# Kernel tuning notes

Hardware: AMD Instinct MI355X
Metric: run time of the kernel (lower is better)

The kernel has to match this reference:

```python
import jax, jax.numpy as jnp
from jax import lax
import numpy as np

DIM = 384
HEADS = 8
MLP_HIDDEN = int(DIM * 4.0)
EPS = 1e-5


def layer_norm(x, g, b):
    m = jnp.mean(x, axis=-1, keepdims=True)
    v = jnp.mean((x - m) ** 2, axis=-1, keepdims=True)
    return (x - m) * lax.rsqrt(v + EPS) * g + b


def conv_pos_enc(x, H, W, w, b):
    # x: (B, N, C) -> depthwise 3x3 conv residual, act=Identity (cpe_act=False)
    B, N, C = x.shape
    feat = jnp.transpose(x, (0, 2, 1)).reshape(B, C, H, W)
    feat = lax.conv_general_dilated(
        feat, w, window_strides=(1, 1), padding='SAME',
        feature_group_count=C, dimension_numbers=('NCHW', 'OIHW', 'NCHW'))
    feat = feat + b[None, :, None, None]
    feat = jnp.transpose(feat.reshape(B, C, N), (0, 2, 1))
    return x + feat


def channel_attn(x, qkv_w, proj_w, proj_b):
    B, N, C = x.shape
    h = HEADS
    hd = C // h
    scale = hd ** (-0.5)
    qkv = x @ qkv_w.T                                # (B, N, 3C)
    qkv = qkv.reshape(B, N, 3, h, hd)
    qkv = jnp.transpose(qkv, (2, 0, 3, 1, 4))        # (3, B, h, N, hd)
    q, k, v = qkv[0], qkv[1], qkv[2]
    k = k * scale
    attn = jnp.einsum('bhnd,bhne->bhde', k, v)       # (B, h, hd, hd)
    attn = jax.nn.softmax(attn, axis=-1)
    out = jnp.einsum('bhde,bhne->bhnd', attn, q)     # (B, h, N, hd)
    out = jnp.transpose(out, (0, 2, 1, 3)).reshape(B, N, C)
    return out @ proj_w.T + proj_b


def mlp(x, fc1_w, fc1_b, fc2_w, fc2_b):
    h = jax.nn.gelu(x @ fc1_w.T + fc1_b, approximate=False)
    return h @ fc2_w.T + fc2_b


def setup_inputs() -> dict:
    key = jax.random.key(0)
    ks = jax.random.split(key, 12)
    C, Hd = DIM, MLP_HIDDEN
    s = 0.02
    return {
        'x': jax.random.normal(ks[0], (32, 784, C), dtype=jnp.float32),
        'H': 28,
        'W': 28,
        'cpe0_w': jax.random.normal(ks[1], (C, 1, 3, 3), dtype=jnp.float32) * s,
        'cpe0_b': jnp.zeros((C,), dtype=jnp.float32),
        'cpe1_w': jax.random.normal(ks[2], (C, 1, 3, 3), dtype=jnp.float32) * s,
        'cpe1_b': jnp.zeros((C,), dtype=jnp.float32),
        'norm1_g': jnp.ones((C,), dtype=jnp.float32),
        'norm1_b': jnp.zeros((C,), dtype=jnp.float32),
        'qkv_w': jax.random.normal(ks[3], (3 * C, C), dtype=jnp.float32) * s,
        'proj_w': jax.random.normal(ks[4], (C, C), dtype=jnp.float32) * s,
        'proj_b': jnp.zeros((C,), dtype=jnp.float32),
        'norm2_g': jnp.ones((C,), dtype=jnp.float32),
        'norm2_b': jnp.zeros((C,), dtype=jnp.float32),
        'fc1_w': jax.random.normal(ks[5], (Hd, C), dtype=jnp.float32) * s,
        'fc1_b': jnp.zeros((Hd,), dtype=jnp.float32),
        'fc2_w': jax.random.normal(ks[6], (C, Hd), dtype=jnp.float32) * s,
        'fc2_b': jnp.zeros((C,), dtype=jnp.float32),
    }


def reference(x, H, W, cpe0_w, cpe0_b, cpe1_w, cpe1_b, norm1_g, norm1_b,
              qkv_w, proj_w, proj_b, norm2_g, norm2_b,
              fc1_w, fc1_b, fc2_w, fc2_b):
    x = conv_pos_enc(x, H, W, cpe0_w, cpe0_b)
    cur = layer_norm(x, norm1_g, norm1_b)
    x = x + channel_attn(cur, qkv_w, proj_w, proj_b)
    x = conv_pos_enc(x, H, W, cpe1_w, cpe1_b)
    x = x + mlp(layer_norm(x, norm2_g, norm2_b), fc1_w, fc1_b, fc2_w, fc2_b)
    return x
```

## Files before the change

kernel.cpp:

```cpp
#include <hip/hip_runtime.h>
#include <hip/hip_bf16.h>
#include <math.h>
#include <stdint.h>

#define B_     32
#define HH_    28
#define WW_    28
#define N_     784
#define C_     384
#define M_     25088
#define HEADS_ 8
#define HD_    48
#define HID_   1536

typedef __bf16 bf16;
typedef __attribute__((ext_vector_type(8))) __bf16 bf16x8;
typedef __attribute__((ext_vector_type(4))) __bf16 bf16x4;
typedef __attribute__((ext_vector_type(4))) float f32x4;

__device__ __forceinline__ void gload_lds16(const void* g, void* l) {
    __builtin_amdgcn_global_load_lds(
        (const __attribute__((address_space(1))) unsigned int*)g,
        (__attribute__((address_space(3))) unsigned int*)(uintptr_t)l,
        16, 0, 0);
}

__device__ __forceinline__ float gelu_f(float v) {
    float u = 0.7978845608028654f * v * (1.f + 0.044715f * v * v);
    return __fdividef(v, 1.f + __expf(-2.f * u));
}

__global__ void convert4_kernel(const float* __restrict__ a, int na,
                                const float* __restrict__ b, int nb,
                                const float* __restrict__ c, int nc,
                                const float* __restrict__ d, int nd,
                                bf16* __restrict__ out) {
    int i = blockIdx.x * 256 + threadIdx.x;
    int j = i;
    const float* src;
    if (j < na) src = a + j;
    else { j -= na;
        if (j < nb) src = b + j;
        else { j -= nb;
            if (j < nc) src = c + j;
            else { j -= nc;
                if (j >= nd) return;
                src = d + j; } } }
    out[i] = (bf16)(*src);
}

__global__ void wtrans_kernel(const float* __restrict__ w0, const float* __restrict__ w1,
                              float* __restrict__ wt0, float* __restrict__ wt1) {
    int i = blockIdx.x * 256 + threadIdx.x;
    if (i >= C_ * 9) return;
    int c = i / 9, t = i - c * 9;
    wt0[t * C_ + c] = w0[i];
    wt1[t * C_ + c] = w1[i];
}

__global__ __launch_bounds__(256)
void cpe_ln_kernel(const float* __restrict__ x, const float* __restrict__ wt,
                   const float* __restrict__ bias, float* __restrict__ y,
                   const float* __restrict__ g, const float* __restrict__ beta,
                   bf16* __restrict__ lnout) {
    const int wave = threadIdx.x >> 6, lane = threadIdx.x & 63;
    const int f = blockIdx.x;
    const int row = (f & 7) * 3136 + (f >> 3) * 4 + wave;
    const int b = row / N_;
    const int n = row - b * N_;
    const int py = n / WW_, px = n - py * WW_;

    float acc[6], ctr[6];
    const float* xrow = x + (size_t)row * C_ + lane;
    #pragma unroll
    for (int j = 0; j < 6; j++) {
        acc[j] = bias[lane + j * 64];
        ctr[j] = xrow[j * 64];
    }

    if (py >= 1 && py <= 26 && px >= 1 && px <= 26) {
        const float* p = x + (size_t)(row - WW_ - 1) * C_ + lane;
        float v[9][6];
        #pragma unroll
        for (int t = 0; t < 9; t++) {
            if (t == 4) continue;
            const float* pt = p + ((t / 3) * WW_ + (t % 3)) * C_;
            #pragma unroll
            for (int j = 0; j < 6; j++) v[t][j] = pt[j * 64];
        }
        #pragma unroll
        for (int t = 0; t < 9; t++) {
            #pragma unroll
            for (int j = 0; j < 6; j++) {
                float xv = (t == 4) ? ctr[j] : v[t][j];
                acc[j] += wt[t * C_ + lane + j * 64] * xv;
            }
        }
    } else {
        #pragma unroll
        for (int t = 0; t < 9; t++) {
            int yy = py + t / 3 - 1, xx = px + t % 3 - 1;
            if (yy < 0 || yy >= HH_ || xx < 0 || xx >= WW_) continue;
            const float* pt = x + (size_t)(b * N_ + yy * WW_ + xx) * C_ + lane;
            #pragma unroll
            for (int j = 0; j < 6; j++)
                acc[j] += wt[t * C_ + lane + j * 64] * pt[j * 64];
        }
    }
    #pragma unroll
    for (int j = 0; j < 6; j++) acc[j] += ctr[j];

    float* yrow = y + (size_t)row * C_ + lane;
    #pragma unroll
    for (int j = 0; j < 6; j++) yrow[j * 64] = acc[j];

    float s = 0.f;
    #pragma unroll
    for (int j = 0; j < 6; j++) s += acc[j];
    #pragma unroll
    for (int off = 1; off < 64; off <<= 1) s += __shfl_xor(s, off, 64);
    float mean = s * (1.f / C_);
    float d[6], vs = 0.f;
    #pragma unroll
    for (int j = 0; j < 6; j++) { d[j] = acc[j] - mean; vs += d[j] * d[j]; }
    #pragma unroll
    for (int off = 1; off < 64; off <<= 1) vs += __shfl_xor(vs, off, 64);
    float rstd = rsqrtf(vs * (1.f / C_) + 1e-5f);
    bf16* lrow = lnout + (size_t)row * C_ + lane;
    #pragma unroll
    for (int j = 0; j < 6; j++) {
        int c = lane + j * 64;
        lrow[j * 64] = (bf16)(d[j] * rstd * g[c] + beta[c]);
    }
}

template<bool BIAS, bool GELU, bool RESID, bool OUTBF>
__global__ __launch_bounds__(256)
void gemm_kernel(const bf16* __restrict__ A, const bf16* __restrict__ Wt,
                 const float* __restrict__ bias, const float* __restrict__ resid,
                 void* __restrict__ outp, int M, int N, int K) {
    __shared__ __align__(16) bf16 As[3 * 4096];
    __shared__ __align__(16) bf16 Bs[3 * 4096];

    const int nbn = gridDim.x, nbm = gridDim.y;
    const int f = blockIdx.y * nbn + blockIdx.x;
    const int grp = f / (8 * nbn);
    const int rem = f - grp * 8 * nbn;
    const int rows = min(8, nbm - grp * 8);
    const int bm = (grp * 8 + rem % rows) * 128;
    const int bn = (rem / rows) * 128;

    const int t = threadIdx.x;
    const int wave = t >> 6, lane = t & 63;
    const int wm = (wave & 1) * 64, wn = (wave >> 1) * 64;
    const int quad = lane >> 4, r = lane & 15;

    const int ldrow = lane >> 2;
    const int ldcol = ((lane & 3) ^ ((lane >> 3) & 3)) * 8;
    const bf16* ga0 = A  + (size_t)(bm + wave * 32 + ldrow) * K + ldcol;
    const bf16* ga1 = ga0 + (size_t)16 * K;
    const bf16* gb0 = Wt + (size_t)(bn + wave * 32 + ldrow) * K + ldcol;
    const bf16* gb1 = gb0 + (size_t)16 * K;
    const int lbase = wave * 1024;
    const int nk = K >> 5;

    auto issue = [&](int st) {
        const int bb = (st % 3) * 4096;
        const int kk = st * 32;
        gload_lds16(ga0 + kk, &As[bb + lbase]);
        gload_lds16(ga1 + kk, &As[bb + lbase + 512]);
        gload_lds16(gb0 + kk, &Bs[bb + lbase]);
        gload_lds16(gb1 + kk, &Bs[bb + lbase + 512]);
    };

    f32x4 acc[4][4] = {};
    issue(0); issue(1);

    const int sq = (quad ^ ((r >> 1) & 3)) * 8;

    for (int s = 0; s < nk; ++s) {
        if (s + 1 < nk) asm volatile("s_waitcnt vmcnt(4)" ::: "memory");
        else            asm volatile("s_waitcnt vmcnt(0)" ::: "memory");
        asm volatile("s_barrier" ::: "memory");
        if (s + 2 < nk) issue(s + 2);

        const bf16* as = &As[(s % 3) * 4096];
        const bf16* bs = &Bs[(s % 3) * 4096];
        bf16x8 af[4], bfr[4];
        #pragma unroll
        for (int i = 0; i < 4; i++)
            af[i] = *(const bf16x8*)(&as[(wm + i * 16 + r) * 32 + sq]);
        #pragma unroll
        for (int j = 0; j < 4; j++)
            bfr[j] = *(const bf16x8*)(&bs[(wn + j * 16 + r) * 32 + sq]);
        #pragma unroll
        for (int i = 0; i < 4; i++)
            #pragma unroll
            for (int j = 0; j < 4; j++)
                acc[i][j] = __builtin_amdgcn_mfma_f32_16x16x32_bf16(bfr[j], af[i], acc[i][j], 0, 0, 0);
    }

    #pragma unroll
    for (int j = 0; j < 4; j++) {
        const int n = bn + wn + j * 16 + quad * 4;
        f32x4 bv = {};
        if (BIAS) bv = *(const f32x4*)(&bias[n]);
        #pragma unroll
        for (int i = 0; i < 4; i++) {
            const size_t m = (size_t)(bm + wm + i * 16 + r);
            f32x4 v = acc[i][j];
            if (BIAS) v += bv;
            if (GELU) {
                #pragma unroll
                for (int e = 0; e < 4; e++) v[e] = gelu_f(v[e]);
            }
            if (RESID) v += *(const f32x4*)(&resid[m * N + n]);
            if (OUTBF) {
                bf16x4 ov;
                #pragma unroll
                for (int e = 0; e < 4; e++) ov[e] = (bf16)v[e];
                *(bf16x4*)((bf16*)outp + m * N + n) = ov;
            } else {
                *(f32x4*)((float*)outp + m * N + n) = v;
            }
        }
    }
}

__global__ __launch_bounds__(256)
void attn_fused_kernel(const bf16* __restrict__ qkvb, bf16* __restrict__ outp) {
    __shared__ __align__(16) bf16 stage[4][3872];
    __shared__ float Sred[4][48][49];
    __shared__ __align__(16) bf16 attn_s[48 * 72];

    const int bh = blockIdx.x;
    const int b = bh >> 3, h = bh & 7;
    const int t = threadIdx.x;
    const int wave = t >> 6, lane = t & 63;
    const int quad = lane >> 4, r = lane & 15;
    const int tensor = lane >> 5;
    const int n_local = lane & 31;

    const size_t qkv_base = (size_t)b * N_ * 1152;
    const int toff = 384 + tensor * 384 + h * 48;

    f32x4 acc[3][3] = {};
    bf16* kT = &stage[wave][0];
    bf16* vT = &stage[wave][1936];
    bf16* myT = &stage[wave][tensor * 1936];

    for (int c = wave; c < 25; c += 4) {
        int n0 = c * 32;
        bf16 rowbuf[48];
        if (n0 + n_local < N_) {
            const uint4* src = (const uint4*)(qkvb + qkv_base + (size_t)(n0 + n_local) * 1152 + toff);
            #pragma unroll
            for (int i = 0; i < 6; i++) *(uint4*)(&rowbuf[i * 8]) = src[i];
        } else {
            #pragma unroll
            for (int i = 0; i < 48; i++) rowbuf[i] = (bf16)0.f;
        }
        #pragma unroll
        for (int d = 0; d < 48; d++) myT[d * 40 + n_local] = rowbuf[d];
        bf16x8 af[3], bfv[3];
        #pragma unroll
        for (int i = 0; i < 3; i++) af[i]  = *(const bf16x8*)(&kT[(i * 16 + r) * 40 + quad * 8]);
        #pragma unroll
        for (int j = 0; j < 3; j++) bfv[j] = *(const bf16x8*)(&vT[(j * 16 + r) * 40 + quad * 8]);
        #pragma unroll
        for (int i = 0; i < 3; i++)
            #pragma unroll
            for (int j = 0; j < 3; j++)
                acc[i][j] = __builtin_amdgcn_mfma_f32_16x16x32_bf16(af[i], bfv[j], acc[i][j], 0, 0, 0);
    }

    #pragma unroll
    for (int i = 0; i < 3; i++)
        #pragma unroll
        for (int j = 0; j < 3; j++)
            #pragma unroll
            for (int e = 0; e < 4; e++)
                Sred[wave][i * 16 + quad * 4 + e][j * 16 + r] = acc[i][j][e];
    __syncthreads();

    if (t < 48) {
        float row[48];
        float mx = -1e30f;
        #pragma unroll
        for (int e = 0; e < 48; e++) {
            float s = Sred[0][t][e] + Sred[1][t][e] + Sred[2][t][e] + Sred[3][t][e];
            s *= 0.14433756729740644f;
            row[e] = s;
            mx = fmaxf(mx, s);
        }
        float sum = 0.f;
        #pragma unroll
        for (int e = 0; e < 48; e++) { float ex = __expf(row[e] - mx); row[e] = ex; sum += ex; }
        float inv = 1.f / sum;
        #pragma unroll
        for (int e = 0; e < 48; e++) attn_s[t * 72 + e] = (bf16)(row[e] * inv);
        #pragma unroll
        for (int e = 48; e < 64; e++) attn_s[t * 72 + e] = (bf16)0.f;
    }
    __syncthreads();

    const bf16* qbase = qkvb + qkv_base + h * 48;
    for (int nt = wave; nt < 49; nt += 4) {
        int n0 = nt * 16;
        f32x4 oacc[3] = {};
        #pragma unroll
        for (int kc = 0; kc < 2; kc++) {
            bf16x8 bq = *(const bf16x8*)(qbase + (size_t)(n0 + r) * 1152 + kc * 32 + quad * 8);
            #pragma unroll
            for (int i = 0; i < 3; i++) {
                bf16x8 aa = *(const bf16x8*)(&attn_s[(i * 16 + r) * 72 + kc * 32 + quad * 8]);
                oacc[i] = __builtin_amdgcn_mfma_f32_16x16x32_bf16(aa, bq, oacc[i], 0, 0, 0);
            }
        }
        #pragma unroll
        for (int i = 0; i < 3; i++) {
            bf16x4 ov;
            #pragma unroll
            for (int e = 0; e < 4; e++) ov[e] = (bf16)oacc[i][e];
            *(bf16x4*)(outp + (size_t)(b * N_ + n0 + r) * 384 + h * 48 + i * 16 + quad * 4) = ov;
        }
    }
}

extern "C" void kernel_launch(void* const* d_in, const int* in_sizes, int n_in,
                              void* d_out, int out_size, void* d_ws, size_t ws_size,
                              hipStream_t stream) {
    const float* x      = (const float*)d_in[0];
    const float* cpe0_w = (const float*)d_in[3];
    const float* cpe0_b = (const float*)d_in[4];
    const float* cpe1_w = (const float*)d_in[5];
    const float* cpe1_b = (const float*)d_in[6];
    const float* n1g    = (const float*)d_in[7];
    const float* n1b    = (const float*)d_in[8];
    const float* qkv_w  = (const float*)d_in[9];
    const float* proj_w = (const float*)d_in[10];
    const float* proj_b = (const float*)d_in[11];
    const float* n2g    = (const float*)d_in[12];
    const float* n2b    = (const float*)d_in[13];
    const float* fc1_w  = (const float*)d_in[14];
    const float* fc1_b  = (const float*)d_in[15];
    const float* fc2_w  = (const float*)d_in[16];
    const float* fc2_b  = (const float*)d_in[17];

    char* ws = (char*)d_ws;
    size_t off = 0;
    bf16* cur    = (bf16*)(ws + off); off += (size_t)M_ * C_ * 2;
    bf16* qkvb   = (bf16*)(ws + off);
    float* x3    = (float*)qkvb;
    off += (size_t)M_ * 1152 * 2;
    bf16* hbuf   = (bf16*)(ws + off); off += (size_t)M_ * HID_ * 2;
    bf16* qkv_wb  = (bf16*)(ws + off); off += (size_t)1152 * 384 * 2;
    bf16* proj_wb = (bf16*)(ws + off); off += (size_t)384 * 384 * 2;
    bf16* fc1_wb  = (bf16*)(ws + off); off += (size_t)HID_ * 384 * 2;
    bf16* fc2_wb  = (bf16*)(ws + off); off += (size_t)384 * HID_ * 2;
    float* wt0    = (float*)(ws + off); off += (size_t)C_ * 9 * 4;
    float* wt1    = (float*)(ws + off); off += (size_t)C_ * 9 * 4;
    float* out = (float*)d_out;

    const int na = 442368, nb = 147456, nc = 589824, nd = 589824;
    convert4_kernel<<<(na + nb + nc + nd + 255) / 256, 256, 0, stream>>>(
        qkv_w, na, proj_w, nb, fc1_w, nc, fc2_w, nd, qkv_wb);
    wtrans_kernel<<<(C_ * 9 + 255) / 256, 256, 0, stream>>>(cpe0_w, cpe1_w, wt0, wt1);

    cpe_ln_kernel<<<M_ / 4, 256, 0, stream>>>(x, wt0, cpe0_b, out, n1g, n1b, cur);
    gemm_kernel<false, false, false, true><<<dim3(1152 / 128, M_ / 128), 256, 0, stream>>>(
        cur, qkv_wb, nullptr, nullptr, qkvb, M_, 1152, 384);
    attn_fused_kernel<<<256, 256, 0, stream>>>(qkvb, cur);
    gemm_kernel<true, false, true, false><<<dim3(384 / 128, M_ / 128), 256, 0, stream>>>(
        cur, proj_wb, proj_b, out, out, M_, 384, 384);
    cpe_ln_kernel<<<M_ / 4, 256, 0, stream>>>(out, wt1, cpe1_b, x3, n2g, n2b, cur);
    gemm_kernel<true, true, false, true><<<dim3(HID_ / 128, M_ / 128), 256, 0, stream>>>(
        cur, fc1_wb, fc1_b, nullptr, hbuf, M_, HID_, 384);
    gemm_kernel<true, false, true, false><<<dim3(384 / 128, M_ / 128), 256, 0, stream>>>(
        hbuf, fc2_wb, fc2_b, x3, out, M_, 384, HID_);
}
```

Measured before the change: 399.8 us.

## Merge weight prep kernels, switch GEMM to double buffering, and rework epilogue

Folds the bf16 weight conversion and the depthwise-weight transpose into one prep kernel, which saves a launch. The GEMM drops from a three-stage to a two-stage LDS pipeline that waits for all loads to land before each step, so less load latency is hidden. The MFMA operand order is swapped and the epilogue now writes scalars instead of 4-wide vectors. The scalar per-element stores and loads are strided, which likely costs bandwidth on the fp32 outputs and residuals.

Measured after the change: 391.0 us. 2.2% less time.

```diff
diff --git a/kernel.cpp b/kernel.cpp
--- a/kernel.cpp
+++ b/kernel.cpp
@@ -30,32 +30,33 @@
     return __fdividef(v, 1.f + __expf(-2.f * u));
 }
 
-__global__ void convert4_kernel(const float* __restrict__ a, int na,
-                                const float* __restrict__ b, int nb,
-                                const float* __restrict__ c, int nc,
-                                const float* __restrict__ d, int nd,
-                                bf16* __restrict__ out) {
+__global__ void prep_kernel(const float* __restrict__ a, int na,
+                            const float* __restrict__ b, int nb,
+                            const float* __restrict__ c, int nc,
+                            const float* __restrict__ d, int nd,
+                            bf16* __restrict__ out,
+                            const float* __restrict__ w0, const float* __restrict__ w1,
+                            float* __restrict__ wt0, float* __restrict__ wt1) {
     int i = blockIdx.x * 256 + threadIdx.x;
-    int j = i;
-    const float* src;
-    if (j < na) src = a + j;
-    else { j -= na;
-        if (j < nb) src = b + j;
-        else { j -= nb;
-            if (j < nc) src = c + j;
-            else { j -= nc;
-                if (j >= nd) return;
-                src = d + j; } } }
-    out[i] = (bf16)(*src);
-}
-
-__global__ void wtrans_kernel(const float* __restrict__ w0, const float* __restrict__ w1,
-                              float* __restrict__ wt0, float* __restrict__ wt1) {
-    int i = blockIdx.x * 256 + threadIdx.x;
-    if (i >= C_ * 9) return;
-    int c = i / 9, t = i - c * 9;
-    wt0[t * C_ + c] = w0[i];
-    wt1[t * C_ + c] = w1[i];
+    const int tot = na + nb + nc + nd;
+    if (i < tot) {
+        int j = i;
+        const float* src;
+        if (j < na) src = a + j;
+        else { j -= na;
+            if (j < nb) src = b + j;
+            else { j -= nb;
+                if (j < nc) src = c + j;
+                else { j -= nc; src = d + j; } } }
+        out[i] = (bf16)(*src);
+    } else {
+        int k = i - tot;
+        if (k < C_ * 9) {
+            int cc = k / 9, tt = k - cc * 9;
+            wt0[tt * C_ + cc] = w0[k];
+            wt1[tt * C_ + cc] = w1[k];
+        }
+    }
 }
 
 __global__ __launch_bounds__(256)
@@ -139,8 +140,8 @@
 void gemm_kernel(const bf16* __restrict__ A, const bf16* __restrict__ Wt,
                  const float* __restrict__ bias, const float* __restrict__ resid,
                  void* __restrict__ outp, int M, int N, int K) {
-    __shared__ __align__(16) bf16 As[3 * 4096];
-    __shared__ __align__(16) bf16 Bs[3 * 4096];
+    __shared__ __align__(16) bf16 As[2 * 4096];
+    __shared__ __align__(16) bf16 Bs[2 * 4096];
 
     const int nbn = gridDim.x, nbm = gridDim.y;
     const int f = blockIdx.y * nbn + blockIdx.x;
@@ -161,11 +162,11 @@
     const bf16* ga1 = ga0 + (size_t)16 * K;
     const bf16* gb0 = Wt + (size_t)(bn + wave * 32 + ldrow) * K + ldcol;
     const bf16* gb1 = gb0 + (size_t)16 * K;
-    const int lbase = wave * 1024;
+    const int lbase = wave * 32 * 32;
     const int nk = K >> 5;
 
     auto issue = [&](int st) {
-        const int bb = (st % 3) * 4096;
+        const int bb = (st & 1) * 4096;
         const int kk = st * 32;
         gload_lds16(ga0 + kk, &As[bb + lbase]);
         gload_lds16(ga1 + kk, &As[bb + lbase + 512]);
@@ -174,18 +175,17 @@
     };
 
     f32x4 acc[4][4] = {};
-    issue(0); issue(1);
+    issue(0);
 
     const int sq = (quad ^ ((r >> 1) & 3)) * 8;
 
     for (int s = 0; s < nk; ++s) {
-        if (s + 1 < nk) asm volatile("s_waitcnt vmcnt(4)" ::: "memory");
-        else            asm volatile("s_waitcnt vmcnt(0)" ::: "memory");
+        asm volatile("s_waitcnt vmcnt(0)" ::: "memory");
         asm volatile("s_barrier" ::: "memory");
-        if (s + 2 < nk) issue(s + 2);
-
-        const bf16* as = &As[(s % 3) * 4096];
-        const bf16* bs = &Bs[(s % 3) * 4096];
+        if (s + 1 < nk) issue(s + 1);
+
+        const bf16* as = &As[(s & 1) * 4096];
+        const bf16* bs = &Bs[(s & 1) * 4096];
         bf16x8 af[4], bfr[4];
         #pragma unroll
         for (int i = 0; i < 4; i++)
@@ -197,31 +197,23 @@
         for (int i = 0; i < 4; i++)
             #pragma unroll
             for (int j = 0; j < 4; j++)
-                acc[i][j] = __builtin_amdgcn_mfma_f32_16x16x32_bf16(bfr[j], af[i], acc[i][j], 0, 0, 0);
-    }
-
-    #pragma unroll
-    for (int j = 0; j < 4; j++) {
-        const int n = bn + wn + j * 16 + quad * 4;
-        f32x4 bv = {};
-        if (BIAS) bv = *(const f32x4*)(&bias[n]);
-        #pragma unroll
-        for (int i = 0; i < 4; i++) {
-            const size_t m = (size_t)(bm + wm + i * 16 + r);
-            f32x4 v = acc[i][j];
-            if (BIAS) v += bv;
-            if (GELU) {
-                #pragma unroll
-                for (int e = 0; e < 4; e++) v[e] = gelu_f(v[e]);
-            }
-            if (RESID) v += *(const f32x4*)(&resid[m * N + n]);
-            if (OUTBF) {
-                bf16x4 ov;
-                #pragma unroll
-                for (int e = 0; e < 4; e++) ov[e] = (bf16)v[e];
-                *(bf16x4*)((bf16*)outp + m * N + n) = ov;
-            } else {
-                *(f32x4*)((float*)outp + m * N + n) = v;
+                acc[i][j] = __builtin_amdgcn_mfma_f32_16x16x32_bf16(af[i], bfr[j], acc[i][j], 0, 0, 0);
+    }
+
+    #pragma unroll
+    for (int i = 0; i < 4; i++) {
+        #pragma unroll
+        for (int j = 0; j < 4; j++) {
+            int n = bn + wn + j * 16 + r;
+            float bv = BIAS ? bias[n] : 0.f;
+            #pragma unroll
+            for (int e = 0; e < 4; e++) {
+                int m = bm + wm + i * 16 + quad * 4 + e;
+                float val = acc[i][j][e] + bv;
+                if (GELU) val = gelu_f(val);
+                if (RESID) val += resid[(size_t)m * N + n];
+                if (OUTBF) ((bf16*)outp)[(size_t)m * N + n] = (bf16)val;
+                else       ((float*)outp)[(size_t)m * N + n] = val;
             }
         }
     }
@@ -363,9 +355,10 @@
     float* out = (float*)d_out;
 
     const int na = 442368, nb = 147456, nc = 589824, nd = 589824;
-    convert4_kernel<<<(na + nb + nc + nd + 255) / 256, 256, 0, stream>>>(
-        qkv_w, na, proj_w, nb, fc1_w, nc, fc2_w, nd, qkv_wb);
-    wtrans_kernel<<<(C_ * 9 + 255) / 256, 256, 0, stream>>>(cpe0_w, cpe1_w, wt0, wt1);
+    const int ntot = na + nb + nc + nd + C_ * 9;
+    prep_kernel<<<(ntot + 255) / 256, 256, 0, stream>>>(
+        qkv_w, na, proj_w, nb, fc1_w, nc, fc2_w, nd, qkv_wb,
+        cpe0_w, cpe1_w, wt0, wt1);
 
     cpe_ln_kernel<<<M_ / 4, 256, 0, stream>>>(x, wt0, cpe0_b, out, n1g, n1b, cur);
     gemm_kernel<false, false, false, true><<<dim3(1152 / 128, M_ / 128), 256, 0, stream>>>(
```
